# Kernel optimization log

Measured on AMD Instinct MI355X. Metric: run time of the kernel, lower is better.

Reference implementation:

```python
import math
import jax, jax.numpy as jnp
import numpy as np

N_EXPERTS = 8
CAP_FACTOR = 1.25
D_MODEL = 1024
D_FF = 4096
B, T = 8, 2048


def setup_inputs() -> dict:
    key = jax.random.key(0)
    k1, k2, k3, k4 = jax.random.split(key, 4)
    hidden = jax.random.normal(k1, (B, T, D_MODEL), dtype=jnp.float32)
    # router: Linear(d_model, n_experts, bias=False), init std=0.01; store as (D, E)
    router_w = jax.random.normal(k2, (D_MODEL, N_EXPERTS), dtype=jnp.float32) * 0.01
    # per-expert MLP weights stacked: W1 (E, D, F), W2 (E, F, D)
    s1 = 1.0 / math.sqrt(D_MODEL)
    s2 = 1.0 / math.sqrt(D_FF)
    W1 = jax.random.uniform(k3, (N_EXPERTS, D_MODEL, D_FF), dtype=jnp.float32, minval=-s1, maxval=s1)
    W2 = jax.random.uniform(k4, (N_EXPERTS, D_FF, D_MODEL), dtype=jnp.float32, minval=-s2, maxval=s2)
    return {"hidden": hidden, "router_w": router_w, "W1": W1, "W2": W2}


def reference(hidden, router_w, W1, W2):
    Bb, Tt, D = hidden.shape
    N = Bb * Tt
    E = router_w.shape[1]
    capacity = min(int(math.ceil(CAP_FACTOR * N / E)), N)

    hidden_flat = hidden.reshape(N, D)
    logits = hidden_flat @ router_w                 # (N, E)
    router_probs = jax.nn.softmax(logits, axis=-1)  # (N, E)

    scores = router_probs.T                         # (E, N)
    weights, indices = jax.lax.top_k(scores, capacity)  # (E, C) each

    # gather tokens per expert: (E, C, D)
    expert_in = hidden_flat[indices]
    h = jnp.einsum('ecd,edf->ecf', expert_in, W1)
    h = jax.nn.gelu(h, approximate=False)           # torch nn.GELU default (erf)
    expert_out = jnp.einsum('ecf,efd->ecd', h, W2)  # (E, C, D)
    contrib = weights[..., None] * expert_out       # (E, C, D)

    output = jnp.zeros((N, D), dtype=hidden.dtype)
    output = output.at[indices.reshape(-1)].add(contrib.reshape(-1, D))
    output = output.reshape(Bb, Tt, D)

    eps = 1e-8
    entropy = -(router_probs * jnp.log(router_probs + eps)).sum(-1)
    aux_loss = -entropy.mean()
    return output, aux_loss
```

## Files before the change

### kernel.cpp

```cpp
#include <hip/hip_runtime.h>
#include <hip/hip_bf16.h>
#include <math.h>

#define NTOK 16384
#define DM 1024
#define DFF 4096
#define NEXP 8
#define CAP 2560

typedef __bf16 bf16;
typedef float f32x4 __attribute__((ext_vector_type(4)));
typedef bf16 bf16x8 __attribute__((ext_vector_type(8)));
typedef bf16 bf16x4 __attribute__((ext_vector_type(4)));

#define OFF_PROBS 0ull
#define OFF_IDX   524288ull
#define OFF_WTS   606208ull
#define OFF_W1T   688128ull
#define OFF_W2T   67796992ull
#define OFF_X     134905856ull
#define OFF_ENT   OFF_X
#define OFF_H     176848896ull
#define WS_MIN    197820416ull
#define WS_FUSED  344621056ull

__device__ __forceinline__ void gl16(const bf16* g, const bf16* l) {
  __builtin_amdgcn_global_load_lds((const __attribute__((address_space(1))) void*)g,
                                   (__attribute__((address_space(3))) void*)l, 16, 0, 0);
}

__device__ __forceinline__ bf16x8 ldsrd16(const bf16* a) {
  bf16x8 d;
  asm volatile("ds_read_b128 %0, %1"
               : "=v"(d)
               : "v"((const __attribute__((address_space(3))) bf16*)a));
  return d;
}

#define LGKM(N) do { asm volatile("s_waitcnt lgkmcnt(%0)" :: "n"(N)); \
                     __builtin_amdgcn_sched_barrier(0); } while (0)

__device__ __forceinline__ float gelu_f(float x) {
  float u = 1.5957691216057308f * (x + 0.044715f * x * x * x);
  return x * __builtin_amdgcn_rcpf(1.f + __expf(-u));
}

__global__ __launch_bounds__(256) void k_transpose_cvt(const float* __restrict__ src,
                                                       bf16* __restrict__ dst, int R, int C) {
  __shared__ float tile[64][69];
  int e = blockIdx.z;
  src += (size_t)e * R * C;
  dst += (size_t)e * R * C;
  int c0 = blockIdx.x * 64, r0 = blockIdx.y * 64;
  int t = threadIdx.x;
  int tr = t >> 4, tc4 = (t & 15) * 4;
#pragma unroll
  for (int i = 0; i < 4; i++) {
    int r = tr + i * 16;
    float4 v = *(const float4*)(src + (size_t)(r0 + r) * C + c0 + tc4);
    tile[r][tc4] = v.x; tile[r][tc4 + 1] = v.y; tile[r][tc4 + 2] = v.z; tile[r][tc4 + 3] = v.w;
  }
  __syncthreads();
#pragma unroll
  for (int i = 0; i < 4; i++) {
    int orr = tr + i * 16;
    bf16x4 o = {(bf16)tile[tc4][orr], (bf16)tile[tc4 + 1][orr],
                (bf16)tile[tc4 + 2][orr], (bf16)tile[tc4 + 3][orr]};
    *(bf16x4*)(dst + (size_t)(c0 + orr) * R + r0 + tc4) = o;
  }
}

__global__ __launch_bounds__(256) void k_router(const float* __restrict__ hidden,
                                                const float* __restrict__ rw,
                                                float* __restrict__ probsT,
                                                float* __restrict__ entPart) {
  __shared__ float went[4];
  int wv = threadIdx.x >> 6, lane = threadIdx.x & 63;
  int token = blockIdx.x * 4 + wv;
  float acc[NEXP];
#pragma unroll
  for (int e = 0; e < NEXP; e++) acc[e] = 0.f;
  const float* hp = hidden + (size_t)token * DM;
  for (int d = lane; d < DM; d += 64) {
    float h = hp[d];
#pragma unroll
    for (int e = 0; e < NEXP; e++) acc[e] = fmaf(h, rw[d * NEXP + e], acc[e]);
  }
#pragma unroll
  for (int e = 0; e < NEXP; e++) {
    float v = acc[e];
#pragma unroll
    for (int s = 1; s < 64; s <<= 1) v += __shfl_xor(v, s);
    acc[e] = v;
  }
  float mx = acc[0];
#pragma unroll
  for (int e = 1; e < NEXP; e++) mx = fmaxf(mx, acc[e]);
  float p[NEXP], s = 0.f;
#pragma unroll
  for (int e = 0; e < NEXP; e++) { p[e] = expf(acc[e] - mx); s += p[e]; }
  float inv = 1.f / s;
  float ent = 0.f;
#pragma unroll
  for (int e = 0; e < NEXP; e++) { p[e] *= inv; ent += p[e] * logf(p[e] + 1e-8f); }
  if (lane < NEXP) probsT[(size_t)lane * NTOK + token] = p[lane];
  if (lane == 0) went[wv] = ent;
  __syncthreads();
  if (threadIdx.x == 0) entPart[blockIdx.x] = went[0] + went[1] + went[2] + went[3];
}

__global__ __launch_bounds__(256) void k_aux(const float* __restrict__ part, float* __restrict__ outAux) {
  __shared__ float s[256];
  int t = threadIdx.x;
  float v = 0.f;
#pragma unroll
  for (int i = 0; i < 16; i++) v += part[i * 256 + t];
  s[t] = v;
  __syncthreads();
  for (int st = 128; st > 0; st >>= 1) {
    if (t < st) s[t] += s[t + st];
    __syncthreads();
  }
  if (t == 0) outAux[0] = s[0] * (1.f / (float)NTOK);
}

__global__ __launch_bounds__(1024) void k_topk(const float* __restrict__ probsT,
                                               int* __restrict__ idx,
                                               float* __restrict__ wts) {
  int e = blockIdx.x;
  const float* row = probsT + (size_t)e * NTOK;
  int t = threadIdx.x;
  unsigned u[16];
#pragma unroll
  for (int j = 0; j < 16; j++) u[j] = __float_as_uint(row[j * 1024 + t]);
  __shared__ int wred[16];
  __shared__ int bc;
  __shared__ int cnt_gt, cnt_eq;
  __shared__ int eqbuf[2048];
  int lane = t & 63, wv = t >> 6;
  unsigned prefix = 0;
  for (int bit = 30; bit >= 0; bit--) {
    unsigned cand = prefix | (1u << bit);
    int c = 0;
#pragma unroll
    for (int j = 0; j < 16; j++) c += (u[j] >= cand) ? 1 : 0;
#pragma unroll
    for (int s = 1; s < 64; s <<= 1) c += __shfl_xor(c, s);
    if (lane == 0) wred[wv] = c;
    __syncthreads();
    if (t == 0) { int tot = 0; for (int k = 0; k < 16; k++) tot += wred[k]; bc = tot; }
    __syncthreads();
    if (bc >= CAP) prefix = cand;
  }
  unsigned vC = prefix;
  if (t == 0) { cnt_gt = 0; cnt_eq = 0; }
  __syncthreads();
#pragma unroll
  for (int j = 0; j < 16; j++) {
    int i = j * 1024 + t;
    if (u[j] > vC) {
      int p = atomicAdd(&cnt_gt, 1);
      idx[e * CAP + p] = i;
      wts[e * CAP + p] = __uint_as_float(u[j]);
    } else if (u[j] == vC) {
      int p = atomicAdd(&cnt_eq, 1);
      if (p < 2048) eqbuf[p] = i;
    }
  }
  __syncthreads();
  int m = cnt_gt;
  int ne = cnt_eq > 2048 ? 2048 : cnt_eq;
  int needed = CAP - m;
  for (int j = t; j < ne; j += 1024) {
    int my = eqbuf[j];
    int rank = 0;
    for (int k = 0; k < ne; k++) rank += (eqbuf[k] < my) ? 1 : 0;
    if (rank < needed) {
      idx[e * CAP + m + rank] = my;
      wts[e * CAP + m + rank] = __uint_as_float(vC);
    }
  }
}

__global__ void k_gather(const float* __restrict__ hidden, const int* __restrict__ idx,
                         bf16* __restrict__ X) {
  int ec = blockIdx.x;
  int token = idx[ec];
  const float4* src = (const float4*)(hidden + (size_t)token * DM);
  bf16* dstrow = X + (size_t)ec * DM;
  int t = threadIdx.x;
  float4 v = src[t];
  bf16x4 o = {(bf16)v.x, (bf16)v.y, (bf16)v.z, (bf16)v.w};
  *(bf16x4*)(dstrow + t * 4) = o;
}

template <int EPI, int BM, int BN, int WMW, int WNW, int NT, int KD>
__global__ __launch_bounds__(512) void k_gemm2ph(
    const bf16* __restrict__ Ab, const bf16* __restrict__ Bb,
    bf16* __restrict__ Hb, const int* __restrict__ idxb, const float* __restrict__ wtsb,
    float* __restrict__ outb, int serialE) {
  constexpr int MF = (BM / WMW) / 16;
  constexpr int NF = (BN / WNW) / 16;
  constexpr int CA = BM / 8;
  constexpr int CB = BN / 8;
  constexpr int S = (CA + CB) / 8;
  constexpr int MT = CAP / BM;

  __shared__ bf16 As[2][BM * 64];
  __shared__ bf16 Bs[2][BN * 64];

  int e, j;
  if (serialE >= 0) { e = serialE; j = blockIdx.x; }
  else { e = blockIdx.x & 7; j = blockIdx.x >> 3; }
  int m0 = (j % MT) * BM;
  int n0 = (j / MT) * BN;

  const bf16* A = Ab + (size_t)e * CAP * KD + (size_t)m0 * KD;
  const bf16* B = Bb + (size_t)e * DFF * DM + (size_t)n0 * KD;

  int t = threadIdx.x, lane = t & 63, wv = t >> 6;
  int wm = wv / WNW, wn = wv % WNW;
  int l3 = lane >> 3, l7 = lane & 7, l15 = lane & 15, khalf = lane >> 4;
  int cswz = (l7 ^ l3) * 8;

  const bf16* gA0 = A + (size_t)l3 * KD + cswz;
  const bf16* gB0 = B + (size_t)l3 * KD + cswz;

  f32x4 acc[MF][NF];
#pragma unroll
  for (int m = 0; m < MF; m++)
#pragma unroll
    for (int n = 0; n < NF; n++) acc[m][n] = (f32x4){0.f, 0.f, 0.f, 0.f};

  auto STAGE = [&](int buf, int ke) {
#pragma unroll
    for (int s = 0; s < S; s++) {
      int c = wv + s * 8;
      if (c < CA) gl16(gA0 + (size_t)(c * 8) * KD + ke, &As[buf][c * 512 + lane * 8]);
      else gl16(gB0 + (size_t)((c - CA) * 8) * KD + ke, &Bs[buf][(c - CA) * 512 + lane * 8]);
    }
  };

  STAGE(0, 0);

  int rowA = wm * (BM / WMW) + l15;
  int rowB = wn * (BN / WNW) + l15;

  for (int kt = 0; kt < NT; kt++) {
    int cur = kt & 1;
    if (kt < NT - 1) {
      STAGE(cur ^ 1, (kt + 1) * 64);
      asm volatile("s_waitcnt vmcnt(%0)" :: "n"(S));
    } else {
      asm volatile("s_waitcnt vmcnt(0)");
    }
    __builtin_amdgcn_s_barrier();

    const char* Ap = (const char*)&As[cur][0];
    const char* Bp = (const char*)&Bs[cur][0];
    int slt0 = ((0 + khalf) ^ l7) * 16;
    int slt1 = ((4 + khalf) ^ l7) * 16;

    {
      bf16x8 aF[MF], bF[NF];
#pragma unroll
      for (int m = 0; m < MF; m++) aF[m] = ldsrd16((const bf16*)(Ap + (rowA + m * 16) * 128 + slt0));
#pragma unroll
      for (int n = 0; n < NF; n++) bF[n] = ldsrd16((const bf16*)(Bp + (rowB + n * 16) * 128 + slt0));
      LGKM(0);
#pragma unroll
      for (int m = 0; m < MF; m++)
#pragma unroll
        for (int n = 0; n < NF; n++)
          acc[m][n] = __builtin_amdgcn_mfma_f32_16x16x32_bf16(aF[m], bF[n], acc[m][n], 0, 0, 0);
    }
    {
      bf16x8 aF[MF], bF[NF];
#pragma unroll
      for (int m = 0; m < MF; m++) aF[m] = ldsrd16((const bf16*)(Ap + (rowA + m * 16) * 128 + slt1));
#pragma unroll
      for (int n = 0; n < NF; n++) bF[n] = ldsrd16((const bf16*)(Bp + (rowB + n * 16) * 128 + slt1));
      LGKM(0);
      __builtin_amdgcn_s_barrier();
#pragma unroll
      for (int m = 0; m < MF; m++)
#pragma unroll
        for (int n = 0; n < NF; n++)
          acc[m][n] = __builtin_amdgcn_mfma_f32_16x16x32_bf16(aF[m], bF[n], acc[m][n], 0, 0, 0);
    }
  }

  int cl = lane & 15, rg = (lane >> 4) * 4;
  if constexpr (EPI == 0) {
    bf16* He = Hb + (size_t)e * CAP * DFF;
#pragma unroll
    for (int m = 0; m < MF; m++) {
      int rowg = m0 + wm * (BM / WMW) + m * 16 + rg;
#pragma unroll
      for (int n = 0; n < NF; n++) {
        int col = n0 + wn * (BN / WNW) + n * 16 + cl;
#pragma unroll
        for (int rr = 0; rr < 4; rr++)
          He[(size_t)(rowg + rr) * DFF + col] = (bf16)gelu_f(acc[m][n][rr]);
      }
    }
  } else {
    const int* idxE = idxb + e * CAP;
    const float* wtsE = wtsb + e * CAP;
#pragma unroll
    for (int m = 0; m < MF; m++) {
      int rowg = m0 + wm * (BM / WMW) + m * 16 + rg;
#pragma unroll
      for (int rr = 0; rr < 4; rr++) {
        int c = rowg + rr;
        int token = idxE[c];
        float w = wtsE[c];
        float* op = outb + (size_t)token * DM + n0 + wn * (BN / WNW) + cl;
#pragma unroll
        for (int n = 0; n < NF; n++) atomicAdd(op + n * 16, w * acc[m][n][rr]);
      }
    }
  }
}

extern "C" void kernel_launch(void* const* d_in, const int* in_sizes, int n_in,
                              void* d_out, int out_size, void* d_ws, size_t ws_size,
                              hipStream_t stream) {
  const float* hidden = (const float*)d_in[0];
  const float* router_w = (const float*)d_in[1];
  const float* W1 = (const float*)d_in[2];
  const float* W2 = (const float*)d_in[3];
  float* out = (float*)d_out;
  if (ws_size < WS_MIN) return;

  char* ws = (char*)d_ws;
  float* probsT = (float*)(ws + OFF_PROBS);
  int* idxb = (int*)(ws + OFF_IDX);
  float* wtsb = (float*)(ws + OFF_WTS);
  bf16* W1T = (bf16*)(ws + OFF_W1T);
  bf16* W2T = (bf16*)(ws + OFF_W2T);
  bf16* Xall = (bf16*)(ws + OFF_X);
  float* entPart = (float*)(ws + OFF_ENT);
  bf16* Hbuf = (bf16*)(ws + OFF_H);

  hipMemsetAsync(d_out, 0, (size_t)out_size * sizeof(float), stream);

  k_transpose_cvt<<<dim3(DFF / 64, DM / 64, NEXP), 256, 0, stream>>>(W1, W1T, DM, DFF);
  k_transpose_cvt<<<dim3(DM / 64, DFF / 64, NEXP), 256, 0, stream>>>(W2, W2T, DFF, DM);

  k_router<<<NTOK / 4, 256, 0, stream>>>(hidden, router_w, probsT, entPart);
  k_aux<<<1, 256, 0, stream>>>(entPart, out + (size_t)NTOK * DM);
  k_topk<<<NEXP, 1024, 0, stream>>>(probsT, idxb, wtsb);
  k_gather<<<NEXP * CAP, 256, 0, stream>>>(hidden, idxb, Xall);

  if (ws_size >= WS_FUSED) {
    k_gemm2ph<0, 256, 256, 2, 4, 16, DM><<<NEXP * 160, 512, 0, stream>>>(
        Xall, W1T, Hbuf, nullptr, nullptr, nullptr, -1);
    k_gemm2ph<1, 320, 256, 2, 4, 64, DFF><<<NEXP * 32, 512, 0, stream>>>(
        Hbuf, W2T, nullptr, idxb, wtsb, out, -1);
  } else {
    for (int e = 0; e < NEXP; e++) {
      bf16* Hadj = Hbuf - (size_t)e * CAP * DFF;
      k_gemm2ph<0, 256, 256, 2, 4, 16, DM><<<160, 512, 0, stream>>>(
          Xall, W1T, Hadj, nullptr, nullptr, nullptr, e);
      k_gemm2ph<1, 320, 256, 2, 4, 64, DFF><<<32, 512, 0, stream>>>(
          Hadj, W2T, nullptr, idxb, wtsb, out, e);
    }
  }
}
```

Measured before the change: 541.1 us.

## Make first expert GEMM persistent with cross-tile prefetch; swap second GEMM warp layout

```diff
diff --git a/kernel.cpp b/kernel.cpp
--- a/kernel.cpp
+++ b/kernel.cpp
@@ -198,7 +198,7 @@
 __global__ __launch_bounds__(512) void k_gemm2ph(
     const bf16* __restrict__ Ab, const bf16* __restrict__ Bb,
     bf16* __restrict__ Hb, const int* __restrict__ idxb, const float* __restrict__ wtsb,
-    float* __restrict__ outb, int serialE) {
+    float* __restrict__ outb, int serialE, int nA) {
   constexpr int MF = (BM / WMW) / 16;
   constexpr int NF = (BN / WNW) / 16;
   constexpr int CA = BM / 8;
@@ -209,22 +209,23 @@
   __shared__ bf16 As[2][BM * 64];
   __shared__ bf16 Bs[2][BN * 64];
 
-  int e, j;
-  if (serialE >= 0) { e = serialE; j = blockIdx.x; }
-  else { e = blockIdx.x & 7; j = blockIdx.x >> 3; }
-  int m0 = (j % MT) * BM;
-  int n0 = (j / MT) * BN;
-
-  const bf16* A = Ab + (size_t)e * CAP * KD + (size_t)m0 * KD;
-  const bf16* B = Bb + (size_t)e * DFF * DM + (size_t)n0 * KD;
+  int e, slot;
+  if (serialE >= 0) { e = serialE; slot = blockIdx.x; }
+  else { e = blockIdx.x & 7; slot = blockIdx.x >> 3; }
+
+  const bf16* Ae = Ab + (size_t)e * CAP * KD;
+  const bf16* Be = Bb + (size_t)e * DFF * DM;
 
   int t = threadIdx.x, lane = t & 63, wv = t >> 6;
   int wm = wv / WNW, wn = wv % WNW;
   int l3 = lane >> 3, l7 = lane & 7, l15 = lane & 15, khalf = lane >> 4;
   int cswz = (l7 ^ l3) * 8;
-
-  const bf16* gA0 = A + (size_t)l3 * KD + cswz;
-  const bf16* gB0 = B + (size_t)l3 * KD + cswz;
+  size_t lofs = (size_t)l3 * KD + cswz;
+
+  int j = slot;
+  int m0 = (j % MT) * BM, n0 = (j / MT) * BN;
+  const bf16* gA0 = Ae + (size_t)m0 * KD + lofs;
+  const bf16* gB0 = Be + (size_t)n0 * KD + lofs;
 
   f32x4 acc[MF][NF];
 #pragma unroll
@@ -232,93 +233,117 @@
 #pragma unroll
     for (int n = 0; n < NF; n++) acc[m][n] = (f32x4){0.f, 0.f, 0.f, 0.f};
 
-  auto STAGE = [&](int buf, int ke) {
+  auto STAGE = [&](const bf16* gA, const bf16* gB, int buf, int ke) {
 #pragma unroll
     for (int s = 0; s < S; s++) {
       int c = wv + s * 8;
-      if (c < CA) gl16(gA0 + (size_t)(c * 8) * KD + ke, &As[buf][c * 512 + lane * 8]);
-      else gl16(gB0 + (size_t)((c - CA) * 8) * KD + ke, &Bs[buf][(c - CA) * 512 + lane * 8]);
+      if (c < CA) gl16(gA + (size_t)(c * 8) * KD + ke, &As[buf][c * 512 + lane * 8]);
+      else gl16(gB + (size_t)((c - CA) * 8) * KD + ke, &Bs[buf][(c - CA) * 512 + lane * 8]);
     }
   };
 
-  STAGE(0, 0);
+  STAGE(gA0, gB0, 0, 0);
 
   int rowA = wm * (BM / WMW) + l15;
   int rowB = wn * (BN / WNW) + l15;
-
-  for (int kt = 0; kt < NT; kt++) {
-    int cur = kt & 1;
-    if (kt < NT - 1) {
-      STAGE(cur ^ 1, (kt + 1) * 64);
-      asm volatile("s_waitcnt vmcnt(%0)" :: "n"(S));
+  int cl = lane & 15, rg = (lane >> 4) * 4;
+
+  for (int a = 0; a < nA; a++) {
+    bool lastA = (a == nA - 1);
+    int m0N = 0, n0N = 0;
+    const bf16 *gA0N = nullptr, *gB0N = nullptr;
+    if (!lastA) {
+      int jn = j + 32;
+      m0N = (jn % MT) * BM; n0N = (jn / MT) * BN;
+      gA0N = Ae + (size_t)m0N * KD + lofs;
+      gB0N = Be + (size_t)n0N * KD + lofs;
+    }
+
+    for (int kt = 0; kt < NT; kt++) {
+      int cur = kt & 1;
+      bool lastT = (kt == NT - 1);
+      if (!lastT) {
+        STAGE(gA0, gB0, cur ^ 1, (kt + 1) * 64);
+        asm volatile("s_waitcnt vmcnt(%0)" :: "n"(S));
+      } else if (!lastA) {
+        STAGE(gA0N, gB0N, cur ^ 1, 0);
+        asm volatile("s_waitcnt vmcnt(%0)" :: "n"(S));
+      } else {
+        asm volatile("s_waitcnt vmcnt(0)");
+      }
+      __builtin_amdgcn_s_barrier();
+
+      const char* Ap = (const char*)&As[cur][0];
+      const char* Bp = (const char*)&Bs[cur][0];
+      int slt0 = ((0 + khalf) ^ l7) * 16;
+      int slt1 = ((4 + khalf) ^ l7) * 16;
+
+      {
+        bf16x8 aF[MF], bF[NF];
+#pragma unroll
+        for (int m = 0; m < MF; m++) aF[m] = ldsrd16((const bf16*)(Ap + (rowA + m * 16) * 128 + slt0));
+#pragma unroll
+        for (int n = 0; n < NF; n++) bF[n] = ldsrd16((const bf16*)(Bp + (rowB + n * 16) * 128 + slt0));
+        LGKM(0);
+#pragma unroll
+        for (int m = 0; m < MF; m++)
+#pragma unroll
+          for (int n = 0; n < NF; n++)
+            acc[m][n] = __builtin_amdgcn_mfma_f32_16x16x32_bf16(aF[m], bF[n], acc[m][n], 0, 0, 0);
+      }
+      {
+        bf16x8 aF[MF], bF[NF];
+#pragma unroll
+        for (int m = 0; m < MF; m++) aF[m] = ldsrd16((const bf16*)(Ap + (rowA + m * 16) * 128 + slt1));
+#pragma unroll
+        for (int n = 0; n < NF; n++) bF[n] = ldsrd16((const bf16*)(Bp + (rowB + n * 16) * 128 + slt1));
+        LGKM(0);
+        __builtin_amdgcn_s_barrier();
+#pragma unroll
+        for (int m = 0; m < MF; m++)
+#pragma unroll
+          for (int n = 0; n < NF; n++)
+            acc[m][n] = __builtin_amdgcn_mfma_f32_16x16x32_bf16(aF[m], bF[n], acc[m][n], 0, 0, 0);
+      }
+    }
+
+    if constexpr (EPI == 0) {
+      bf16* He = Hb + (size_t)e * CAP * DFF;
+#pragma unroll
+      for (int m = 0; m < MF; m++) {
+        int rowg = m0 + wm * (BM / WMW) + m * 16 + rg;
+#pragma unroll
+        for (int n = 0; n < NF; n++) {
+          int col = n0 + wn * (BN / WNW) + n * 16 + cl;
+#pragma unroll
+          for (int rr = 0; rr < 4; rr++)
+            He[(size_t)(rowg + rr) * DFF + col] = (bf16)gelu_f(acc[m][n][rr]);
+        }
+      }
     } else {
-      asm volatile("s_waitcnt vmcnt(0)");
-    }
-    __builtin_amdgcn_s_barrier();
-
-    const char* Ap = (const char*)&As[cur][0];
-    const char* Bp = (const char*)&Bs[cur][0];
-    int slt0 = ((0 + khalf) ^ l7) * 16;
-    int slt1 = ((4 + khalf) ^ l7) * 16;
-
-    {
-      bf16x8 aF[MF], bF[NF];
-#pragma unroll
-      for (int m = 0; m < MF; m++) aF[m] = ldsrd16((const bf16*)(Ap + (rowA + m * 16) * 128 + slt0));
-#pragma unroll
-      for (int n = 0; n < NF; n++) bF[n] = ldsrd16((const bf16*)(Bp + (rowB + n * 16) * 128 + slt0));
-      LGKM(0);
+      const int* idxE = idxb + e * CAP;
+      const float* wtsE = wtsb + e * CAP;
+#pragma unroll
+      for (int m = 0; m < MF; m++) {
+        int rowg = m0 + wm * (BM / WMW) + m * 16 + rg;
+#pragma unroll
+        for (int rr = 0; rr < 4; rr++) {
+          int c = rowg + rr;
+          int token = idxE[c];
+          float w = wtsE[c];
+          float* op = outb + (size_t)token * DM + n0 + wn * (BN / WNW) + cl;
+#pragma unroll
+          for (int n = 0; n < NF; n++) atomicAdd(op + n * 16, w * acc[m][n][rr]);
+        }
+      }
+    }
+
+    if (!lastA) {
+      j += 32; m0 = m0N; n0 = n0N; gA0 = gA0N; gB0 = gB0N;
 #pragma unroll
       for (int m = 0; m < MF; m++)
 #pragma unroll
-        for (int n = 0; n < NF; n++)
-          acc[m][n] = __builtin_amdgcn_mfma_f32_16x16x32_bf16(aF[m], bF[n], acc[m][n], 0, 0, 0);
-    }
-    {
-      bf16x8 aF[MF], bF[NF];
-#pragma unroll
-      for (int m = 0; m < MF; m++) aF[m] = ldsrd16((const bf16*)(Ap + (rowA + m * 16) * 128 + slt1));
-#pragma unroll
-      for (int n = 0; n < NF; n++) bF[n] = ldsrd16((const bf16*)(Bp + (rowB + n * 16) * 128 + slt1));
-      LGKM(0);
-      __builtin_amdgcn_s_barrier();
-#pragma unroll
-      for (int m = 0; m < MF; m++)
-#pragma unroll
-        for (int n = 0; n < NF; n++)
-          acc[m][n] = __builtin_amdgcn_mfma_f32_16x16x32_bf16(aF[m], bF[n], acc[m][n], 0, 0, 0);
-    }
-  }
-
-  int cl = lane & 15, rg = (lane >> 4) * 4;
-  if constexpr (EPI == 0) {
-    bf16* He = Hb + (size_t)e * CAP * DFF;
-#pragma unroll
-    for (int m = 0; m < MF; m++) {
-      int rowg = m0 + wm * (BM / WMW) + m * 16 + rg;
-#pragma unroll
-      for (int n = 0; n < NF; n++) {
-        int col = n0 + wn * (BN / WNW) + n * 16 + cl;
-#pragma unroll
-        for (int rr = 0; rr < 4; rr++)
-          He[(size_t)(rowg + rr) * DFF + col] = (bf16)gelu_f(acc[m][n][rr]);
-      }
-    }
-  } else {
-    const int* idxE = idxb + e * CAP;
-    const float* wtsE = wtsb + e * CAP;
-#pragma unroll
-    for (int m = 0; m < MF; m++) {
-      int rowg = m0 + wm * (BM / WMW) + m * 16 + rg;
-#pragma unroll
-      for (int rr = 0; rr < 4; rr++) {
-        int c = rowg + rr;
-        int token = idxE[c];
-        float w = wtsE[c];
-        float* op = outb + (size_t)token * DM + n0 + wn * (BN / WNW) + cl;
-#pragma unroll
-        for (int n = 0; n < NF; n++) atomicAdd(op + n * 16, w * acc[m][n][rr]);
-      }
+        for (int n = 0; n < NF; n++) acc[m][n] = (f32x4){0.f, 0.f, 0.f, 0.f};
     }
   }
 }
@@ -354,17 +379,17 @@
   k_gather<<<NEXP * CAP, 256, 0, stream>>>(hidden, idxb, Xall);
 
   if (ws_size >= WS_FUSED) {
-    k_gemm2ph<0, 256, 256, 2, 4, 16, DM><<<NEXP * 160, 512, 0, stream>>>(
-        Xall, W1T, Hbuf, nullptr, nullptr, nullptr, -1);
-    k_gemm2ph<1, 320, 256, 2, 4, 64, DFF><<<NEXP * 32, 512, 0, stream>>>(
-        Hbuf, W2T, nullptr, idxb, wtsb, out, -1);
+    k_gemm2ph<0, 256, 256, 2, 4, 16, DM><<<256, 512, 0, stream>>>(
+        Xall, W1T, Hbuf, nullptr, nullptr, nullptr, -1, 5);
+    k_gemm2ph<1, 320, 256, 4, 2, 64, DFF><<<256, 512, 0, stream>>>(
+        Hbuf, W2T, nullptr, idxb, wtsb, out, -1, 1);
   } else {
     for (int e = 0; e < NEXP; e++) {
       bf16* Hadj = Hbuf - (size_t)e * CAP * DFF;
       k_gemm2ph<0, 256, 256, 2, 4, 16, DM><<<160, 512, 0, stream>>>(
-          Xall, W1T, Hadj, nullptr, nullptr, nullptr, e);
-      k_gemm2ph<1, 320, 256, 2, 4, 64, DFF><<<32, 512, 0, stream>>>(
-          Hadj, W2T, nullptr, idxb, wtsb, out, e);
-    }
-  }
-}
+          Xall, W1T, Hadj, nullptr, nullptr, nullptr, e, 1);
+      k_gemm2ph<1, 320, 256, 4, 2, 64, DFF><<<32, 512, 0, stream>>>(
+          Hadj, W2T, nullptr, idxb, wtsb, out, e, 1);
+    }
+  }
+}
```

New measurement: 547.1 us. About the same (+1.1%).
